# Kernel tuning notes

Measured on AMD Instinct MI355X. Metric: run time of the kernel, lower is better.

Reference implementation:

```python
import jax, jax.numpy as jnp
import numpy as np

N_NODES = 50000


def gcn_conv(x, W, b, src, dst):
    # PyG GCNConv: lin (no bias) -> add self-loops -> symmetric deg norm ->
    # scatter-add messages to target nodes -> add bias.
    n = x.shape[0]
    xw = x @ W  # [N, H]
    loops = jnp.arange(n, dtype=src.dtype)
    s = jnp.concatenate([src, loops])
    d = jnp.concatenate([dst, loops])
    deg = jax.ops.segment_sum(jnp.ones(d.shape[0], dtype=x.dtype), d, num_segments=n)
    dinv = deg ** -0.5  # deg >= 1 due to self-loops
    norm = dinv[s] * dinv[d]  # [E+N]
    msg = xw[s] * norm[:, None]  # gather + scale, [E+N, H]
    out = jax.ops.segment_sum(msg, d, num_segments=n)  # scatter-add
    return out + b


def setup_inputs() -> dict:
    key = jax.random.key(0)
    ks = jax.random.split(key, 8)
    in_feats, hidden, out_feats, p = 64, 64, 32, 4
    x = jax.random.normal(ks[0], (N_NODES, in_feats), dtype=jnp.float32)
    edge_index = jax.random.randint(ks[1], (2, 800000), 0, N_NODES, dtype=jnp.int64)
    s1 = (1.0 / in_feats) ** 0.5
    s2 = (1.0 / hidden) ** 0.5
    W1 = jax.random.uniform(ks[2], (in_feats, hidden), jnp.float32, -s1, s1)
    b1 = jnp.zeros((hidden,), jnp.float32)
    W2 = jax.random.uniform(ks[3], (hidden, hidden), jnp.float32, -s2, s2)
    b2 = jnp.zeros((hidden,), jnp.float32)
    Wr = jax.random.uniform(ks[4], (hidden, out_feats * p), jnp.float32, -s2, s2)
    br = jax.random.uniform(ks[5], (out_feats * p,), jnp.float32, -s2, s2)
    return {"x": x, "edge_index": edge_index, "W1": W1, "b1": b1,
            "W2": W2, "b2": b2, "Wr": Wr, "br": br}


def reference(x, edge_index, W1, b1, W2, b2, Wr, br):
    src, dst = edge_index[0], edge_index[1]
    h = jax.nn.relu(gcn_conv(x, W1, b1, src, dst))
    h = jax.nn.relu(gcn_conv(h, W2, b2, src, dst))
    g = jnp.mean(h, axis=0, keepdims=True)  # [1, hidden]
    out = (g @ Wr + br).reshape(32, 4)  # (out_feats, p)
    return out
```

## Files before the change

### kernel.cpp

```cpp
#include <hip/hip_runtime.h>
#include <math.h>


#define HID 64

__global__ void k_hist(const int* __restrict__ dst, int* __restrict__ counts, int E) {
    int e = blockIdx.x * blockDim.x + threadIdx.x;
    if (e < E) atomicAdd(&counts[dst[e]], 1);
}

__global__ void k_blocksum(const int* __restrict__ counts, int* __restrict__ bsum, int n) {
    __shared__ int sm[256];
    int t = threadIdx.x;
    int i = blockIdx.x * 256 + t;
    sm[t] = (i < n) ? counts[i] : 0;
    __syncthreads();
    for (int off = 128; off > 0; off >>= 1) {
        if (t < off) sm[t] += sm[t + off];
        __syncthreads();
    }
    if (t == 0) bsum[blockIdx.x] = sm[0];
}

__global__ void k_scanb(const int* __restrict__ bsum, int* __restrict__ boff, int nb) {
    __shared__ int sm[256];
    int t = threadIdx.x;
    int v = (t < nb) ? bsum[t] : 0;
    sm[t] = v;
    __syncthreads();
    for (int off = 1; off < 256; off <<= 1) {
        int x = (t >= off) ? sm[t - off] : 0;
        __syncthreads();
        sm[t] += x;
        __syncthreads();
    }
    if (t < nb) boff[t] = sm[t] - v;
}

__global__ void k_finalize(const int* __restrict__ counts, const int* __restrict__ boff,
                           int* __restrict__ offsets, int* __restrict__ cursor,
                           float* __restrict__ dinv, int n, int E) {
    __shared__ int sm[256];
    int t = threadIdx.x;
    int i = blockIdx.x * 256 + t;
    int v = (i < n) ? counts[i] : 0;
    sm[t] = v;
    __syncthreads();
    for (int off = 1; off < 256; off <<= 1) {
        int x = (t >= off) ? sm[t - off] : 0;
        __syncthreads();
        sm[t] += x;
        __syncthreads();
    }
    if (i < n) {
        int excl = boff[blockIdx.x] + sm[t] - v;
        offsets[i] = excl;
        cursor[i] = excl;
        dinv[i] = 1.0f / sqrtf((float)(v + 1));
        if (i == n - 1) offsets[n] = E;
    }
}

__global__ void k_scatter(const int* __restrict__ src, const int* __restrict__ dst,
                          int* __restrict__ cursor, int* __restrict__ csr_src, int E) {
    int e = blockIdx.x * blockDim.x + threadIdx.x;
    if (e < E) {
        int pos = atomicAdd(&cursor[dst[e]], 1);
        csr_src[pos] = src[e];
    }
}

__global__ __launch_bounds__(256) void k_gemm_scale(const float* __restrict__ X,
                                                    const float* __restrict__ W,
                                                    const float* __restrict__ dinv,
                                                    float* __restrict__ Y, int n) {
    __shared__ float Ws[64 * 64];
    __shared__ float xs[16][64];
    int t = threadIdx.x, w = t >> 6, f = t & 63;
    const float4* W4 = (const float4*)W;
    float4* Ws4 = (float4*)Ws;
#pragma unroll
    for (int j = 0; j < 4; j++) Ws4[t + 256 * j] = W4[t + 256 * j];
    int r0 = blockIdx.x * 16;
#pragma unroll
    for (int i = 0; i < 4; i++) {
        int r = r0 + w * 4 + i;
        xs[w * 4 + i][f] = (r < n) ? X[(size_t)r * 64 + f] : 0.f;
    }
    __syncthreads();
    float acc[4] = {0.f, 0.f, 0.f, 0.f};
#pragma unroll 8
    for (int k = 0; k < 64; k++) {
        float wv = Ws[k * 64 + f];
#pragma unroll
        for (int i = 0; i < 4; i++) acc[i] += xs[w * 4 + i][k] * wv;
    }
#pragma unroll
    for (int i = 0; i < 4; i++) {
        int r = r0 + w * 4 + i;
        if (r < n) Y[(size_t)r * 64 + f] = dinv[r] * acc[i];
    }
}

template <bool POOL>
__global__ __launch_bounds__(256) void k_aggregate(const float* __restrict__ Y,
                                                   const float* __restrict__ dinv,
                                                   const float* __restrict__ bias,
                                                   const int* __restrict__ offsets,
                                                   const int* __restrict__ csr_src,
                                                   float* __restrict__ H,
                                                   float* __restrict__ pbuf, int n) {
    __shared__ float sm[256];
    int t = threadIdx.x, w = t >> 6, f = t & 63;
    int node = blockIdx.x * 4 + w;
    bool valid = node < n;
    float hval = 0.f;
    if (valid) {
        int beg = offsets[node], end = offsets[node + 1];
        float acc = Y[(size_t)node * 64 + f];
        for (int j = beg; j < end; j += 8) {
#pragma unroll
            for (int u = 0; u < 8; u++) {
                int jj = j + u;
                bool c = jj < end;
                int jc = c ? jj : beg;
                int s = csr_src[jc];
                float a = Y[(size_t)s * 64 + f];
                acc += c ? a : 0.f;
            }
        }
        hval = fmaxf(dinv[node] * acc + bias[f], 0.f);
        if (!POOL) H[(size_t)node * 64 + f] = hval;
    }
    if (POOL) {
        sm[t] = valid ? hval : 0.f;
        __syncthreads();
        if (w == 0) pbuf[(size_t)blockIdx.x * 64 + f] =
            sm[f] + sm[64 + f] + sm[128 + f] + sm[192 + f];
    }
}

__global__ void k_mean_final(const float* __restrict__ pbuf, float* __restrict__ g,
                             int nrows) {
    __shared__ float part[256];
    int t = threadIdx.x, w = t >> 6, f = t & 63;
    float local = 0.f;
    for (int r = blockIdx.x * 4 + w; r < nrows; r += gridDim.x * 4)
        local += pbuf[(size_t)r * 64 + f];
    part[t] = local;
    __syncthreads();
    if (w == 0) {
        float tot = part[f] + part[64 + f] + part[128 + f] + part[192 + f];
        atomicAdd(&g[f], tot);
    }
}

__global__ void k_readout(const float* __restrict__ g, const float* __restrict__ Wr,
                          const float* __restrict__ br, float* __restrict__ out,
                          float invn) {
    __shared__ float gl[64];
    int t = threadIdx.x;
    if (t < 64) gl[t] = g[t] * invn;
    __syncthreads();
    float acc = br[t];
#pragma unroll
    for (int k = 0; k < 64; k++) acc += gl[k] * Wr[k * 128 + t];
    out[t] = acc;
}

extern "C" void kernel_launch(void* const* d_in, const int* in_sizes, int n_in,
                              void* d_out, int out_size, void* d_ws, size_t ws_size,
                              hipStream_t stream) {
    const float* x  = (const float*)d_in[0];
    const int*   ei = (const int*)d_in[1];
    const float* W1 = (const float*)d_in[2];
    const float* b1 = (const float*)d_in[3];
    const float* W2 = (const float*)d_in[4];
    const float* b2 = (const float*)d_in[5];
    const float* Wr = (const float*)d_in[6];
    const float* br = (const float*)d_in[7];
    float* out = (float*)d_out;

    int n = in_sizes[0] / 64;
    int E = in_sizes[1] / 2;
    const int* src = ei;
    const int* dst = ei + E;

    char* p = (char*)d_ws;
    float* y = (float*)p;      p += (size_t)n * 64 * sizeof(float);
    float* h = (float*)p;      p += (size_t)n * 64 * sizeof(float);
    float* dinv = (float*)p;   p += (size_t)n * sizeof(float);
    float* g = (float*)p;      p += 64 * sizeof(float);
    int* counts = (int*)p;     p += (size_t)n * sizeof(int);
    int* offsets = (int*)p;    p += (size_t)(n + 1) * sizeof(int);
    int* cursor = (int*)p;     p += (size_t)n * sizeof(int);
    int* bsum = (int*)p;       p += 256 * sizeof(int);
    int* boff = (int*)p;       p += 256 * sizeof(int);
    int* csr_src = (int*)p;    p += (size_t)E * sizeof(int);

    int nb = (n + 255) / 256;
    int eb = (E + 255) / 256;
    int gb = (n + 3) / 4;

    hipMemsetAsync(counts, 0, (size_t)n * sizeof(int), stream);
    hipMemsetAsync(g, 0, 64 * sizeof(float), stream);
    k_hist<<<eb, 256, 0, stream>>>(dst, counts, E);
    k_blocksum<<<nb, 256, 0, stream>>>(counts, bsum, n);
    k_scanb<<<1, 256, 0, stream>>>(bsum, boff, nb);
    k_finalize<<<nb, 256, 0, stream>>>(counts, boff, offsets, cursor, dinv, n, E);
    k_scatter<<<eb, 256, 0, stream>>>(src, dst, cursor, csr_src, E);

    k_gemm_scale<<<(n + 15) / 16, 256, 0, stream>>>(x, W1, dinv, y, n);
    k_aggregate<false><<<gb, 256, 0, stream>>>(y, dinv, b1, offsets, csr_src, h, nullptr, n);
    k_gemm_scale<<<(n + 15) / 16, 256, 0, stream>>>(h, W2, dinv, y, n);
    float* pbuf = h;
    k_aggregate<true><<<gb, 256, 0, stream>>>(y, dinv, b2, offsets, csr_src, nullptr, pbuf, n);

    k_mean_final<<<64, 256, 0, stream>>>(pbuf, g, gb);
    k_readout<<<1, 128, 0, stream>>>(g, Wr, br, out, 1.0f / (float)n);
}
```

Measured before the change: 274.9 us.

## Replace per-node CSR build with 64-node bucket sort and shared-memory aggregation

Edges are no longer sorted into a full per-node CSR with global atomics. They are partitioned into buckets of 64 destination nodes using per-chunk shared-memory histograms, one scan, and a scatter that packs (src<<6 | local dst) into a single int. Degree and aggregation then work per bucket, accumulating messages in a 64x64 shared-memory tile with LDS atomics. This is meant to cut the cost of global atomic contention in graph construction, at the price of LDS atomics during aggregation and a single-block serial scan over the histogram matrix.

```diff
diff --git a/kernel.cpp b/kernel.cpp
--- a/kernel.cpp
+++ b/kernel.cpp
@@ -2,72 +2,100 @@
 #include <math.h>
 
 
-#define HID 64
-
-__global__ void k_hist(const int* __restrict__ dst, int* __restrict__ counts, int E) {
-    int e = blockIdx.x * blockDim.x + threadIdx.x;
-    if (e < E) atomicAdd(&counts[dst[e]], 1);
-}
-
-__global__ void k_blocksum(const int* __restrict__ counts, int* __restrict__ bsum, int n) {
-    __shared__ int sm[256];
-    int t = threadIdx.x;
-    int i = blockIdx.x * 256 + t;
-    sm[t] = (i < n) ? counts[i] : 0;
-    __syncthreads();
-    for (int off = 128; off > 0; off >>= 1) {
-        if (t < off) sm[t] += sm[t + off];
-        __syncthreads();
-    }
-    if (t == 0) bsum[blockIdx.x] = sm[0];
-}
-
-__global__ void k_scanb(const int* __restrict__ bsum, int* __restrict__ boff, int nb) {
-    __shared__ int sm[256];
-    int t = threadIdx.x;
-    int v = (t < nb) ? bsum[t] : 0;
-    sm[t] = v;
-    __syncthreads();
-    for (int off = 1; off < 256; off <<= 1) {
-        int x = (t >= off) ? sm[t - off] : 0;
-        __syncthreads();
-        sm[t] += x;
-        __syncthreads();
-    }
-    if (t < nb) boff[t] = sm[t] - v;
-}
-
-__global__ void k_finalize(const int* __restrict__ counts, const int* __restrict__ boff,
-                           int* __restrict__ offsets, int* __restrict__ cursor,
-                           float* __restrict__ dinv, int n, int E) {
-    __shared__ int sm[256];
-    int t = threadIdx.x;
-    int i = blockIdx.x * 256 + t;
-    int v = (i < n) ? counts[i] : 0;
-    sm[t] = v;
-    __syncthreads();
-    for (int off = 1; off < 256; off <<= 1) {
-        int x = (t >= off) ? sm[t - off] : 0;
-        __syncthreads();
-        sm[t] += x;
-        __syncthreads();
-    }
-    if (i < n) {
-        int excl = boff[blockIdx.x] + sm[t] - v;
-        offsets[i] = excl;
-        cursor[i] = excl;
-        dinv[i] = 1.0f / sqrtf((float)(v + 1));
-        if (i == n - 1) offsets[n] = E;
-    }
-}
-
-__global__ void k_scatter(const int* __restrict__ src, const int* __restrict__ dst,
-                          int* __restrict__ cursor, int* __restrict__ csr_src, int E) {
-    int e = blockIdx.x * blockDim.x + threadIdx.x;
-    if (e < E) {
-        int pos = atomicAdd(&cursor[dst[e]], 1);
-        csr_src[pos] = src[e];
-    }
+#define CH 16384
+#define MAXNB 1024
+
+__global__ __launch_bounds__(256) void k_bucket_hist(const int* __restrict__ dst,
+                                                     int* __restrict__ histmat,
+                                                     int E, int NB, int nch) {
+    __shared__ int ih[MAXNB];
+    int t = threadIdx.x;
+    for (int k = t; k < NB; k += 256) ih[k] = 0;
+    __syncthreads();
+    int base = blockIdx.x * CH;
+    for (int i = 0; i < CH; i += 256) {
+        int e = base + i + t;
+        if (e < E) atomicAdd(&ih[dst[e] >> 6], 1);
+    }
+    __syncthreads();
+    for (int k = t; k < NB; k += 256) histmat[(size_t)k * nch + blockIdx.x] = ih[k];
+}
+
+__global__ __launch_bounds__(256) void k_scan(int* __restrict__ histmat,
+                                              int* __restrict__ bstart,
+                                              int NB, int nch, int E) {
+    __shared__ int tot[MAXNB];
+    __shared__ int sc[256];
+    __shared__ int carry;
+    int t = threadIdx.x;
+    for (int k = t; k < NB; k += 256) {
+        int s = 0;
+        const int* row = histmat + (size_t)k * nch;
+        for (int b = 0; b < nch; b++) s += row[b];
+        tot[k] = s;
+    }
+    if (t == 0) carry = 0;
+    __syncthreads();
+    int nchunk = (NB + 255) / 256;
+    for (int c = 0; c < nchunk; c++) {
+        int idx = c * 256 + t;
+        int v = (idx < NB) ? tot[idx] : 0;
+        sc[t] = v;
+        __syncthreads();
+        for (int off = 1; off < 256; off <<= 1) {
+            int x = (t >= off) ? sc[t - off] : 0;
+            __syncthreads();
+            sc[t] += x;
+            __syncthreads();
+        }
+        int excl = sc[t] - v + carry;
+        if (idx < NB) tot[idx] = excl;
+        __syncthreads();
+        if (t == 0) carry += sc[255];
+        __syncthreads();
+    }
+    for (int k = t; k < NB; k += 256) {
+        int base = tot[k];
+        bstart[k] = base;
+        int* row = histmat + (size_t)k * nch;
+        for (int b = 0; b < nch; b++) { int tmp = row[b]; row[b] = base; base += tmp; }
+    }
+    if (t == 0) bstart[NB] = E;
+}
+
+__global__ __launch_bounds__(256) void k_bucket_scatter(const int* __restrict__ src,
+                                                        const int* __restrict__ dst,
+                                                        const int* __restrict__ histmat,
+                                                        int* __restrict__ staged,
+                                                        int E, int NB, int nch) {
+    __shared__ int cur[MAXNB];
+    int t = threadIdx.x;
+    for (int k = t; k < NB; k += 256) cur[k] = histmat[(size_t)k * nch + blockIdx.x];
+    __syncthreads();
+    int base = blockIdx.x * CH;
+    for (int i = 0; i < CH; i += 256) {
+        int e = base + i + t;
+        if (e < E) {
+            int d = dst[e];
+            int pos = atomicAdd(&cur[d >> 6], 1);
+            staged[pos] = (src[e] << 6) | (d & 63);
+        }
+    }
+}
+
+__global__ __launch_bounds__(256) void k_deg_dinv(const int* __restrict__ staged,
+                                                  const int* __restrict__ bstart,
+                                                  float* __restrict__ dinv, int n) {
+    __shared__ int degl[64];
+    int t = threadIdx.x;
+    if (t < 64) degl[t] = 0;
+    __syncthreads();
+    int k = blockIdx.x;
+    int beg = bstart[k], end = bstart[k + 1];
+    for (int e = beg + t; e < end; e += 256) atomicAdd(&degl[staged[e] & 63], 1);
+    __syncthreads();
+    int node = k * 64 + t;
+    if (t < 64 && node < n) dinv[node] = 1.0f / sqrtf((float)(degl[t] + 1));
 }
 
 __global__ __launch_bounds__(256) void k_gemm_scale(const float* __restrict__ X,
@@ -103,40 +131,55 @@
 }
 
 template <bool POOL>
-__global__ __launch_bounds__(256) void k_aggregate(const float* __restrict__ Y,
-                                                   const float* __restrict__ dinv,
-                                                   const float* __restrict__ bias,
-                                                   const int* __restrict__ offsets,
-                                                   const int* __restrict__ csr_src,
-                                                   float* __restrict__ H,
-                                                   float* __restrict__ pbuf, int n) {
-    __shared__ float sm[256];
+__global__ __launch_bounds__(256) void k_bucket_aggregate(const float* __restrict__ Y,
+                                                          const float* __restrict__ dinv,
+                                                          const float* __restrict__ bias,
+                                                          const int* __restrict__ staged,
+                                                          const int* __restrict__ bstart,
+                                                          float* __restrict__ H,
+                                                          float* __restrict__ pbuf, int n) {
+    __shared__ float acc[64 * 64];
     int t = threadIdx.x, w = t >> 6, f = t & 63;
-    int node = blockIdx.x * 4 + w;
-    bool valid = node < n;
-    float hval = 0.f;
-    if (valid) {
-        int beg = offsets[node], end = offsets[node + 1];
-        float acc = Y[(size_t)node * 64 + f];
-        for (int j = beg; j < end; j += 8) {
-#pragma unroll
-            for (int u = 0; u < 8; u++) {
-                int jj = j + u;
-                bool c = jj < end;
-                int jc = c ? jj : beg;
-                int s = csr_src[jc];
-                float a = Y[(size_t)s * 64 + f];
-                acc += c ? a : 0.f;
+    float4* a4 = (float4*)acc;
+    for (int i = t; i < 1024; i += 256) a4[i] = make_float4(0.f, 0.f, 0.f, 0.f);
+    __syncthreads();
+    int k = blockIdx.x;
+    int beg = bstart[k], end = bstart[k + 1];
+    for (int e0 = beg + w * 8; e0 < end; e0 += 32) {
+#pragma unroll
+        for (int u = 0; u < 8; u++) {
+            int e = e0 + u;
+            bool c = e < end;
+            int pk = staged[c ? e : beg];
+            int s = pk >> 6, dl = pk & 63;
+            float v = Y[(size_t)s * 64 + f];
+            if (c) atomicAdd(&acc[dl * 64 + f], v);
+        }
+    }
+    __syncthreads();
+    int node0 = k * 64;
+    if (!POOL) {
+        for (int nl = w; nl < 64; nl += 4) {
+            int node = node0 + nl;
+            if (node < n) {
+                float v = acc[nl * 64 + f] + Y[(size_t)node * 64 + f];
+                H[(size_t)node * 64 + f] = fmaxf(dinv[node] * v + bias[f], 0.f);
             }
         }
-        hval = fmaxf(dinv[node] * acc + bias[f], 0.f);
-        if (!POOL) H[(size_t)node * 64 + f] = hval;
-    }
-    if (POOL) {
-        sm[t] = valid ? hval : 0.f;
-        __syncthreads();
-        if (w == 0) pbuf[(size_t)blockIdx.x * 64 + f] =
-            sm[f] + sm[64 + f] + sm[128 + f] + sm[192 + f];
+    } else {
+        float psum = 0.f;
+        for (int nl = w; nl < 64; nl += 4) {
+            int node = node0 + nl;
+            if (node < n) {
+                float v = acc[nl * 64 + f] + Y[(size_t)node * 64 + f];
+                psum += fmaxf(dinv[node] * v + bias[f], 0.f);
+            }
+        }
+        __syncthreads();
+        acc[t] = psum;
+        __syncthreads();
+        if (w == 0) pbuf[(size_t)k * 64 + f] =
+            acc[f] + acc[64 + f] + acc[128 + f] + acc[192 + f];
     }
 }
 
@@ -186,36 +229,30 @@
     const int* src = ei;
     const int* dst = ei + E;
 
+    int NB  = (n + 63) / 64;
+    int nch = (E + CH - 1) / CH;
+
     char* p = (char*)d_ws;
     float* y = (float*)p;      p += (size_t)n * 64 * sizeof(float);
     float* h = (float*)p;      p += (size_t)n * 64 * sizeof(float);
     float* dinv = (float*)p;   p += (size_t)n * sizeof(float);
     float* g = (float*)p;      p += 64 * sizeof(float);
-    int* counts = (int*)p;     p += (size_t)n * sizeof(int);
-    int* offsets = (int*)p;    p += (size_t)(n + 1) * sizeof(int);
-    int* cursor = (int*)p;     p += (size_t)n * sizeof(int);
-    int* bsum = (int*)p;       p += 256 * sizeof(int);
-    int* boff = (int*)p;       p += 256 * sizeof(int);
-    int* csr_src = (int*)p;    p += (size_t)E * sizeof(int);
-
-    int nb = (n + 255) / 256;
-    int eb = (E + 255) / 256;
-    int gb = (n + 3) / 4;
-
-    hipMemsetAsync(counts, 0, (size_t)n * sizeof(int), stream);
+    int* staged = (int*)p;     p += (size_t)E * sizeof(int);
+    int* histmat = (int*)p;    p += (size_t)NB * nch * sizeof(int);
+    int* bstart = (int*)p;     p += (size_t)(NB + 1) * sizeof(int);
+
     hipMemsetAsync(g, 0, 64 * sizeof(float), stream);
-    k_hist<<<eb, 256, 0, stream>>>(dst, counts, E);
-    k_blocksum<<<nb, 256, 0, stream>>>(counts, bsum, n);
-    k_scanb<<<1, 256, 0, stream>>>(bsum, boff, nb);
-    k_finalize<<<nb, 256, 0, stream>>>(counts, boff, offsets, cursor, dinv, n, E);
-    k_scatter<<<eb, 256, 0, stream>>>(src, dst, cursor, csr_src, E);
+    k_bucket_hist<<<nch, 256, 0, stream>>>(dst, histmat, E, NB, nch);
+    k_scan<<<1, 256, 0, stream>>>(histmat, bstart, NB, nch, E);
+    k_bucket_scatter<<<nch, 256, 0, stream>>>(src, dst, histmat, staged, E, NB, nch);
+    k_deg_dinv<<<NB, 256, 0, stream>>>(staged, bstart, dinv, n);
 
     k_gemm_scale<<<(n + 15) / 16, 256, 0, stream>>>(x, W1, dinv, y, n);
-    k_aggregate<false><<<gb, 256, 0, stream>>>(y, dinv, b1, offsets, csr_src, h, nullptr, n);
+    k_bucket_aggregate<false><<<NB, 256, 0, stream>>>(y, dinv, b1, staged, bstart, h, nullptr, n);
     k_gemm_scale<<<(n + 15) / 16, 256, 0, stream>>>(h, W2, dinv, y, n);
     float* pbuf = h;
-    k_aggregate<true><<<gb, 256, 0, stream>>>(y, dinv, b2, offsets, csr_src, nullptr, pbuf, n);
-
-    k_mean_final<<<64, 256, 0, stream>>>(pbuf, g, gb);
+    k_bucket_aggregate<true><<<NB, 256, 0, stream>>>(y, dinv, b2, staged, bstart, nullptr, pbuf, n);
+
+    k_mean_final<<<64, 256, 0, stream>>>(pbuf, g, NB);
     k_readout<<<1, 128, 0, stream>>>(g, Wr, br, out, 1.0f / (float)n);
 }
```

New measurement: 953.2 us. +246.8%, slower.
